# Performance work log

Measured on AMD Instinct MI355X. Metric: run time of the kernel, lower is better.

Reference implementation:

```python
import jax, jax.numpy as jnp
import numpy as np
from itertools import permutations as _permutations

N_ORB = 64
N_ALPHA = 5
N_BETA = 5
TEMP = 1.0
PERMS5 = jnp.asarray(np.array(list(_permutations(range(5))), dtype=np.int32))  # (120, 5)


def setup_inputs() -> dict:
    key = jax.random.key(0)
    ks = jax.random.split(key, 16)
    B = 8192
    s = 0.02
    inp = {
        "uniform_alpha": jax.random.uniform(ks[0], (B, N_ORB), dtype=jnp.float32),
        "uniform_beta": jax.random.uniform(ks[1], (B, N_ORB), dtype=jnp.float32),
        # learnable params
        "alpha_logits": jax.random.normal(ks[2], (N_ORB,), dtype=jnp.float32) * s,
        # alpha_to_beta: Linear(n_orb,128) -> SiLU -> Linear(128,64)
        "W1": jax.random.normal(ks[3], (N_ORB, 128), dtype=jnp.float32) * s,
        "b1": jnp.zeros((128,), jnp.float32),
        "W2": jax.random.normal(ks[4], (128, 64), dtype=jnp.float32) * s,
        "b2": jnp.zeros((64,), jnp.float32),
        # beta_conditioned_scorer: Linear(n_orb+64,256)->SiLU->Linear(256,256)->SiLU->Linear(256,n_orb)
        "V1": jax.random.normal(ks[5], (N_ORB + 64, 256), dtype=jnp.float32) * s,
        "c1": jnp.zeros((256,), jnp.float32),
        "V2": jax.random.normal(ks[6], (256, 256), dtype=jnp.float32) * s,
        "c2": jnp.zeros((256,), jnp.float32),
        "V3": jax.random.normal(ks[7], (256, N_ORB), dtype=jnp.float32) * s,
        "c3": jnp.zeros((N_ORB,), jnp.float32),
    }
    return inp


def _gumbel_topk(logits, uniform, k):
    """Straight-through Gumbel top-k mask. logits, uniform: (B, n)."""
    g = -jnp.log(-jnp.log(jnp.maximum(uniform, 1e-10)))
    perturbed = (logits + g) / TEMP
    _, top_idx = jax.lax.top_k(perturbed, k)                      # (B, k)
    B = logits.shape[0]
    one_hot = jnp.zeros_like(logits).at[jnp.arange(B)[:, None], top_idx].set(1.0)
    soft = jax.nn.softmax(perturbed, axis=-1)
    return one_hot - jax.lax.stop_gradient(soft) + soft


def _exact_pl_log_prob(logits, selection, k, perms):
    """log P(unordered top-k set) under Plackett-Luce, exact over k! orderings.

    logits: (B, n); selection: (B, n) soft/hard mask; perms: (P, k) static.
    """
    B, n = logits.shape
    P = perms.shape[0]
    _, sel_idx = jax.lax.top_k(selection, k)
    sel_idx = jnp.sort(sel_idx, axis=-1)                          # (B, k)
    perm_idx = sel_idx[:, perms]                                  # (B, P, k)
    lg = logits[:, None, :]                                       # (B, 1, n)
    remaining = jnp.ones((B, P, n), dtype=bool)
    lp = jnp.zeros((B, P), logits.dtype)
    bi = jnp.arange(B)[:, None]
    pi = jnp.arange(P)[None, :]
    for step in range(k):  # k is small and static (5)
        masked = jnp.where(remaining, lg, -jnp.inf)
        logp = jax.nn.log_softmax(masked, axis=-1)                # (B, P, n)
        idx = perm_idx[:, :, step]                                # (B, P)
        lp = lp + jnp.take_along_axis(logp, idx[..., None], axis=-1)[..., 0]
        remaining = remaining.at[bi, pi, idx].set(False)
    return jax.scipy.special.logsumexp(lp, axis=-1)              # (B,)


def reference(uniform_alpha, uniform_beta, alpha_logits, W1, b1, W2, b2,
              V1, c1, V2, c2, V3, c3):
    B = uniform_alpha.shape[0]
    a_logits = jnp.broadcast_to(alpha_logits[None, :], (B, N_ORB))
    alpha_config = _gumbel_topk(a_logits, uniform_alpha, N_ALPHA)

    # alpha_to_beta MLP
    h = jax.nn.silu(alpha_config @ W1 + b1)
    alpha_context = h @ W2 + b2                                   # (B, 64)

    beta_input = jnp.concatenate([jnp.zeros((B, N_ORB), a_logits.dtype), alpha_context], axis=-1)
    z = jax.nn.silu(beta_input @ V1 + c1)
    z = jax.nn.silu(z @ V2 + c2)
    beta_logits = z @ V3 + c3                                     # (B, n_orb)

    beta_config = _gumbel_topk(beta_logits, uniform_beta, N_BETA)
    configs = jnp.concatenate([alpha_config, beta_config], axis=-1)

    lp_a = _exact_pl_log_prob(a_logits, alpha_config, N_ALPHA, PERMS5)
    lp_b = _exact_pl_log_prob(beta_logits, beta_config, N_BETA, PERMS5)
    log_probs = lp_a + lp_b
    return configs, log_probs
```

## Files before the change

kernel.cpp:

```cpp
#include <hip/hip_runtime.h>
#include <math.h>

#define NTH 1024
#define KP 264
#define SPB 16
#define OFF_W2 0
#define OFF_V1 16384
#define OFF_V2 49152
#define OFF_V3 180224
#define WS_USHORTS 212992
#define MFMA16 __builtin_amdgcn_mfma_f32_16x16x32_bf16

typedef __attribute__((ext_vector_type(8))) short s16x8;
typedef __attribute__((ext_vector_type(8))) unsigned short u16x8;
typedef __attribute__((ext_vector_type(4))) float f32x4;

__device__ __forceinline__ float waveSum(float v) {
#pragma unroll
  for (int off = 32; off; off >>= 1) v += __shfl_xor(v, off, 64);
  return v;
}

__device__ __forceinline__ float siluf(float x) { return x / (1.0f + expf(-x)); }

__device__ __forceinline__ unsigned short bround(float x) {
  unsigned u = __float_as_uint(x);
  return (unsigned short)((u + 0x7FFFu + ((u >> 16) & 1u)) >> 16);
}

__device__ __forceinline__ void bsplit(float x, unsigned short& h, unsigned short& l) {
  unsigned u = __float_as_uint(x);
  unsigned hb = (u + 0x7FFFu + ((u >> 16) & 1u)) >> 16;
  float hf = __uint_as_float(hb << 16);
  float lf = x - hf;
  unsigned ul = __float_as_uint(lf);
  unsigned lb = (ul + 0x7FFFu + ((ul >> 16) & 1u)) >> 16;
  h = (unsigned short)hb; l = (unsigned short)lb;
}

__device__ __forceinline__ float permSum(const float se0, const float se1,
                                         const float se2, const float se3,
                                         const float se4, float Z, int lane) {
  float psum = 0.0f;
#pragma unroll
  for (int pp = 0; pp < 2; ++pp) {
    int p = lane + pp * 64;
    if (p < 120) {
      int rem = p;
      unsigned avail = 0x43210u;
      float c = 0.0f;
      float prod = Z;
#pragma unroll
      for (int j = 0; j < 4; ++j) {
        const int fct = (j == 0) ? 24 : (j == 1) ? 6 : (j == 2) ? 2 : 1;
        int q = rem / fct; rem -= q * fct;
        int sh = q * 4;
        int dg = (avail >> sh) & 0xF;
        avail = (avail & ((1u << sh) - 1u)) | ((avail >> (sh + 4)) << sh);
        float ev = (dg == 0) ? se0 : (dg == 1) ? se1 : (dg == 2) ? se2
                 : (dg == 3) ? se3 : se4;
        c += ev;
        prod *= (Z - c);
      }
      psum += 1.0f / prod;
    }
  }
  return psum;
}

__device__ __forceinline__ float selectAndPL(float lv, float ev, float Z,
                                             const float* __restrict__ u64,
                                             float* __restrict__ gout,
                                             int lane,
                                             float* __restrict__ sValsRow,
                                             float* __restrict__ sSelERow,
                                             int* __restrict__ selIdxRow) {
  float u = u64[lane];
  float g = -logf(-logf(fmaxf(u, 1e-10f)));
  float v = lv + g;
  sValsRow[lane] = v;
  int rank = 0;
#pragma unroll
  for (int j = 0; j < 16; ++j) {
    float4 w = *(const float4*)&sValsRow[j * 4];
    int base = j * 4;
    rank += (w.x > v || (w.x == v && base + 0 < lane)) ? 1 : 0;
    rank += (w.y > v || (w.y == v && base + 1 < lane)) ? 1 : 0;
    rank += (w.z > v || (w.z == v && base + 2 < lane)) ? 1 : 0;
    rank += (w.w > v || (w.w == v && base + 3 < lane)) ? 1 : 0;
  }
  bool sel = rank < 5;
  gout[lane] = sel ? 1.0f : 0.0f;
  if (sel) {
    sSelERow[rank] = ev;
    if (selIdxRow) selIdxRow[rank] = lane;
  }
  float sl = waveSum(sel ? lv : 0.0f);
  float se0 = sSelERow[0], se1 = sSelERow[1], se2 = sSelERow[2],
        se3 = sSelERow[3], se4 = sSelERow[4];
  float S = waveSum(permSum(se0, se1, se2, se3, se4, Z, lane));
  return sl + logf(S);
}

__global__ __launch_bounds__(256)
void pcf_prep(const float* __restrict__ W2, const float* __restrict__ V1,
              const float* __restrict__ V2, const float* __restrict__ V3,
              unsigned short* __restrict__ ws)
{
  int tid = blockIdx.x * 256 + threadIdx.x;
  const float* src; int N, Ks, dstoff, r;
  if (tid < 1024)       { src = W2;            N = 64;  Ks = 4; dstoff = OFF_W2; r = tid; }
  else if (tid < 3072)  { src = V1 + 64 * 256; N = 256; Ks = 2; dstoff = OFF_V1; r = tid - 1024; }
  else if (tid < 11264) { src = V2;            N = 256; Ks = 8; dstoff = OFF_V2; r = tid - 3072; }
  else                  { src = V3;            N = 64;  Ks = 8; dstoff = OFF_V3; r = tid - 11264; }
  int lane = r & 63, ts = r >> 6;
  int ks = ts % Ks, ct = ts / Ks;
  int n = ct * 16 + (lane & 15);
  int k0 = ks * 32 + (lane >> 4) * 8;
  u16x8 hv, lv;
#pragma unroll
  for (int j = 0; j < 8; ++j) {
    float x = src[(size_t)(k0 + j) * N + n];
    unsigned short h, l;
    bsplit(x, h, l);
    hv[j] = h; lv[j] = l;
  }
  unsigned short* dst = ws + dstoff + (size_t)ts * 1024 + lane * 8;
  *(u16x8*)dst = hv;
  *(u16x8*)(dst + 512) = lv;
}

__global__ __launch_bounds__(NTH, 8)
void pcf_mfma(const float* __restrict__ ua, const float* __restrict__ ub,
              const float* __restrict__ alog, const float* __restrict__ W1,
              const float* __restrict__ b1, const float* __restrict__ b2,
              const float* __restrict__ c1, const float* __restrict__ c2,
              const float* __restrict__ c3,
              const unsigned short* __restrict__ wt, float* __restrict__ out)
{
  __shared__ unsigned short sAhi[16 * KP];
  __shared__ unsigned short sBhi[16 * KP];
  __shared__ float sBL[SPB * 64];
  __shared__ float sVals[16 * 64];
  __shared__ float sSelE[16 * 8];
  __shared__ int   sSelA[SPB * 5];
  __shared__ float sLpA[SPB];

  const int t    = threadIdx.x;
  const int lane = t & 63;
  const int wv   = t >> 6;
  const int ln15 = lane & 15;
  const int quad = lane >> 4;
  const int bbase = blockIdx.x * SPB;

  float* sValsRow = &sVals[wv * 64];
  float* sSelERow = &sSelE[wv * 8];

  {
    float la = alog[lane];
    float ea = expf(la);
    float Za = waveSum(ea);
    int b = bbase + wv;
    float lp = selectAndPL(la, ea, Za, ua + (size_t)b * 64,
                           out + (size_t)b * 128, lane,
                           sValsRow, sSelERow, &sSelA[wv * 5]);
    if (lane == 0) sLpA[wv] = lp;
  }
  __syncthreads();

  {
    int s = wv;
    int j = lane * 2;
    const int rows[5] = { sSelA[s * 5 + 0], sSelA[s * 5 + 1], sSelA[s * 5 + 2],
                          sSelA[s * 5 + 3], sSelA[s * 5 + 4] };
    float2 a = *(const float2*)(b1 + j);
#pragma unroll
    for (int r = 0; r < 5; ++r) {
      float2 w = *(const float2*)(W1 + (size_t)rows[r] * 128 + j);
      a.x += w.x; a.y += w.y;
    }
    unsigned h0 = bround(siluf(a.x));
    unsigned h1 = bround(siluf(a.y));
    *(unsigned*)&sAhi[s * KP + j] = h0 | (h1 << 16);
  }
  __syncthreads();

  if (wv < 4) {
    f32x4 acc = {0.f, 0.f, 0.f, 0.f};
#pragma unroll
    for (int ks = 0; ks < 4; ++ks) {
      int ko = ks * 32 + quad * 8;
      s16x8 ah = *(const s16x8*)&sAhi[ln15 * KP + ko];
      const unsigned short* tsb = wt + OFF_W2 + (size_t)(wv * 4 + ks) * 1024;
      s16x8 bh = ((const s16x8*)tsb)[lane];
      s16x8 bl = ((const s16x8*)(tsb + 512))[lane];
      acc = MFMA16(ah, bh, acc, 0, 0, 0);
      acc = MFMA16(ah, bl, acc, 0, 0, 0);
    }
    int col = wv * 16 + ln15;
    float bias = b2[col];
#pragma unroll
    for (int r = 0; r < 4; ++r)
      sBhi[(quad * 4 + r) * KP + col] = bround(acc[r] + bias);
  }
  __syncthreads();

  {
    f32x4 acc = {0.f, 0.f, 0.f, 0.f};
#pragma unroll
    for (int ks = 0; ks < 2; ++ks) {
      int ko = ks * 32 + quad * 8;
      s16x8 ah = *(const s16x8*)&sBhi[ln15 * KP + ko];
      const unsigned short* tsb = wt + OFF_V1 + (size_t)(wv * 2 + ks) * 1024;
      s16x8 bh = ((const s16x8*)tsb)[lane];
      s16x8 bl = ((const s16x8*)(tsb + 512))[lane];
      acc = MFMA16(ah, bh, acc, 0, 0, 0);
      acc = MFMA16(ah, bl, acc, 0, 0, 0);
    }
    int col = wv * 16 + ln15;
    float bias = c1[col];
#pragma unroll
    for (int r = 0; r < 4; ++r)
      sAhi[(quad * 4 + r) * KP + col] = bround(siluf(acc[r] + bias));
  }
  __syncthreads();

  {
    f32x4 acc = {0.f, 0.f, 0.f, 0.f};
#pragma unroll 4
    for (int ks = 0; ks < 8; ++ks) {
      int ko = ks * 32 + quad * 8;
      s16x8 ah = *(const s16x8*)&sAhi[ln15 * KP + ko];
      const unsigned short* tsb = wt + OFF_V2 + (size_t)(wv * 8 + ks) * 1024;
      s16x8 bh = ((const s16x8*)tsb)[lane];
      s16x8 bl = ((const s16x8*)(tsb + 512))[lane];
      acc = MFMA16(ah, bh, acc, 0, 0, 0);
      acc = MFMA16(ah, bl, acc, 0, 0, 0);
    }
    int col = wv * 16 + ln15;
    float bias = c2[col];
#pragma unroll
    for (int r = 0; r < 4; ++r)
      sBhi[(quad * 4 + r) * KP + col] = bround(siluf(acc[r] + bias));
  }
  __syncthreads();

  if (wv < 4) {
    f32x4 acc = {0.f, 0.f, 0.f, 0.f};
#pragma unroll
    for (int ks = 0; ks < 8; ++ks) {
      int ko = ks * 32 + quad * 8;
      s16x8 ah = *(const s16x8*)&sBhi[ln15 * KP + ko];
      const unsigned short* tsb = wt + OFF_V3 + (size_t)(wv * 8 + ks) * 1024;
      s16x8 bh = ((const s16x8*)tsb)[lane];
      s16x8 bl = ((const s16x8*)(tsb + 512))[lane];
      acc = MFMA16(ah, bh, acc, 0, 0, 0);
      acc = MFMA16(ah, bl, acc, 0, 0, 0);
    }
    int col = wv * 16 + ln15;
    float bias = c3[col];
#pragma unroll
    for (int r = 0; r < 4; ++r)
      sBL[(quad * 4 + r) * 64 + col] = acc[r] + bias;
  }
  __syncthreads();

  {
    int b = bbase + wv;
    float blv = sBL[wv * 64 + lane];
    float eb = expf(blv);
    float Zb = waveSum(eb);
    float lp = selectAndPL(blv, eb, Zb, ub + (size_t)b * 64,
                           out + (size_t)b * 128 + 64, lane,
                           sValsRow, sSelERow, nullptr);
    if (lane == 0)
      out[(size_t)8192 * 128 + b] = sLpA[wv] + lp;
  }
}

#define SPB4 4
__global__ __launch_bounds__(256, 8)
void pcf_small(const float* __restrict__ ua, const float* __restrict__ ub,
               const float* __restrict__ alog, const float* __restrict__ W1,
               const float* __restrict__ b1, const float* __restrict__ W2,
               const float* __restrict__ b2, const float* __restrict__ V1,
               const float* __restrict__ c1, const float* __restrict__ V2,
               const float* __restrict__ c2, const float* __restrict__ V3,
               const float* __restrict__ c3, float* __restrict__ out)
{
  __shared__ float sA[SPB4 * 256];
  __shared__ float sB[SPB4 * 256];
  __shared__ float sP[4 * 256];
  __shared__ float sVals[4 * 64];
  __shared__ float sSelE[4 * 8];
  __shared__ int   sSelA[SPB4 * 5];
  __shared__ float sLpA[SPB4];

  const int t    = threadIdx.x;
  const int lane = t & 63;
  const int wv   = t >> 6;
  const int bbase = blockIdx.x * SPB4;

  float* sValsRow = &sVals[wv * 64];
  float* sSelERow = &sSelE[wv * 8];

  {
    float la = alog[lane];
    float ea = expf(la);
    float Za = waveSum(ea);
    int b = bbase + wv;
    float lp = selectAndPL(la, ea, Za, ua + (size_t)b * 64,
                           out + (size_t)b * 128, lane,
                           sValsRow, sSelERow, &sSelA[wv * 5]);
    if (lane == 0) sLpA[wv] = lp;
  }
  __syncthreads();
  {
    int s = wv;
    int i0 = sSelA[s * 5 + 0], i1 = sSelA[s * 5 + 1], i2 = sSelA[s * 5 + 2];
    int i3 = sSelA[s * 5 + 3], i4 = sSelA[s * 5 + 4];
#pragma unroll
    for (int jh = 0; jh < 2; ++jh) {
      int j = lane + jh * 64;
      float acc = b1[j] + W1[i0 * 128 + j] + W1[i1 * 128 + j]
                + W1[i2 * 128 + j] + W1[i3 * 128 + j] + W1[i4 * 128 + j];
      sA[s * 128 + j] = siluf(acc);
    }
  }
  __syncthreads();
  {
    float acc[SPB4] = {};
    const int kb = 32 * wv;
#pragma unroll 2
    for (int m = 0; m < 8; ++m) {
      int k0 = kb + 4 * m;
      float w0 = W2[(k0 + 0) * 64 + lane];
      float w1 = W2[(k0 + 1) * 64 + lane];
      float w2 = W2[(k0 + 2) * 64 + lane];
      float w3 = W2[(k0 + 3) * 64 + lane];
#pragma unroll
      for (int s = 0; s < SPB4; ++s) {
        float4 x = *(float4*)&sA[s * 128 + k0];
        acc[s] += x.x * w0 + x.y * w1 + x.z * w2 + x.w * w3;
      }
    }
#pragma unroll
    for (int s = 0; s < SPB4; ++s) sP[wv * 256 + s * 64 + lane] = acc[s];
  }
  __syncthreads();
  {
    int o = t;
    float v = b2[o & 63] + sP[o] + sP[256 + o] + sP[512 + o] + sP[768 + o];
    sB[o] = v;
  }
  __syncthreads();
  {
    const int c = 64 * wv + lane;
    float acc[SPB4];
    float cb = c1[c];
#pragma unroll
    for (int s = 0; s < SPB4; ++s) acc[s] = cb;
    const float* wp = V1 + (size_t)64 * 256 + c;
#pragma unroll 4
    for (int m = 0; m < 16; ++m) {
      int k0 = 4 * m;
      float w0 = wp[(k0 + 0) * 256];
      float w1 = wp[(k0 + 1) * 256];
      float w2 = wp[(k0 + 2) * 256];
      float w3 = wp[(k0 + 3) * 256];
#pragma unroll
      for (int s = 0; s < SPB4; ++s) {
        float4 x = *(float4*)&sB[s * 64 + k0];
        acc[s] += x.x * w0 + x.y * w1 + x.z * w2 + x.w * w3;
      }
    }
#pragma unroll
    for (int s = 0; s < SPB4; ++s) sA[s * 256 + c] = siluf(acc[s]);
  }
  __syncthreads();
  {
    const int c = 64 * wv + lane;
    float acc[SPB4];
    float cb = c2[c];
#pragma unroll
    for (int s = 0; s < SPB4; ++s) acc[s] = cb;
    const float* wp = V2 + c;
#pragma unroll 4
    for (int m = 0; m < 64; ++m) {
      int k0 = 4 * m;
      float w0 = wp[(size_t)(k0 + 0) * 256];
      float w1 = wp[(size_t)(k0 + 1) * 256];
      float w2 = wp[(size_t)(k0 + 2) * 256];
      float w3 = wp[(size_t)(k0 + 3) * 256];
#pragma unroll
      for (int s = 0; s < SPB4; ++s) {
        float4 x = *(float4*)&sA[s * 256 + k0];
        acc[s] += x.x * w0 + x.y * w1 + x.z * w2 + x.w * w3;
      }
    }
#pragma unroll
    for (int s = 0; s < SPB4; ++s) sB[s * 256 + c] = siluf(acc[s]);
  }
  __syncthreads();
  {
    float acc[SPB4] = {};
    const int kb = 64 * wv;
#pragma unroll 4
    for (int m = 0; m < 16; ++m) {
      int k0 = kb + 4 * m;
      float w0 = V3[(k0 + 0) * 64 + lane];
      float w1 = V3[(k0 + 1) * 64 + lane];
      float w2 = V3[(k0 + 2) * 64 + lane];
      float w3 = V3[(k0 + 3) * 64 + lane];
#pragma unroll
      for (int s = 0; s < SPB4; ++s) {
        float4 x = *(float4*)&sB[s * 256 + k0];
        acc[s] += x.x * w0 + x.y * w1 + x.z * w2 + x.w * w3;
      }
    }
#pragma unroll
    for (int s = 0; s < SPB4; ++s) sP[wv * 256 + s * 64 + lane] = acc[s];
  }
  __syncthreads();
  {
    int b = bbase + wv;
    float blv = c3[lane] + sP[wv * 64 + lane] + sP[256 + wv * 64 + lane]
              + sP[512 + wv * 64 + lane] + sP[768 + wv * 64 + lane];
    float eb = expf(blv);
    float Zb = waveSum(eb);
    float lp = selectAndPL(blv, eb, Zb, ub + (size_t)b * 64,
                           out + (size_t)b * 128 + 64, lane,
                           sValsRow, sSelERow, nullptr);
    if (lane == 0)
      out[(size_t)8192 * 128 + b] = sLpA[wv] + lp;
  }
}

extern "C" void kernel_launch(void* const* d_in, const int* in_sizes, int n_in,
                              void* d_out, int out_size, void* d_ws, size_t ws_size,
                              hipStream_t stream) {
  const float* ua   = (const float*)d_in[0];
  const float* ub   = (const float*)d_in[1];
  const float* alog = (const float*)d_in[2];
  const float* W1   = (const float*)d_in[3];
  const float* b1   = (const float*)d_in[4];
  const float* W2   = (const float*)d_in[5];
  const float* b2   = (const float*)d_in[6];
  const float* V1   = (const float*)d_in[7];
  const float* c1   = (const float*)d_in[8];
  const float* V2   = (const float*)d_in[9];
  const float* c2   = (const float*)d_in[10];
  const float* V3   = (const float*)d_in[11];
  const float* c3   = (const float*)d_in[12];
  float* out = (float*)d_out;

  if (ws_size >= (size_t)WS_USHORTS * 2) {
    unsigned short* wt = (unsigned short*)d_ws;
    pcf_prep<<<dim3(52), dim3(256), 0, stream>>>(W2, V1, V2, V3, wt);
    pcf_mfma<<<dim3(8192 / SPB), dim3(NTH), 0, stream>>>(
        ua, ub, alog, W1, b1, b2, c1, c2, c3, wt, out);
  } else {
    pcf_small<<<dim3(8192 / SPB4), dim3(256), 0, stream>>>(
        ua, ub, alog, W1, b1, W2, b2, V1, c1, V2, c2, V3, c3, out);
  }
}
```

Baseline: 108.3 us.

## Halve block to 512 threads, two samples per wave, prefetch beta uniforms

The MFMA kernel's block drops from 16 to 8 waves. Each wave now handles two samples in the selection stages and two 16-column tiles in the V1 and V2 GEMM stages. The beta uniforms are loaded and their Gumbel noise computed at kernel start, so that global load latency overlaps the MLP work. This cuts per-block barrier cost and lets more blocks share a CU, but each wave carries more serial work and more registers. The W2 and V3 stages still use wv<4, which now means half of the 8 waves.

```diff
diff --git a/kernel.cpp b/kernel.cpp
--- a/kernel.cpp
+++ b/kernel.cpp
@@ -1,7 +1,7 @@
 #include <hip/hip_runtime.h>
 #include <math.h>
 
-#define NTH 1024
+#define NTH 512
 #define KP 264
 #define SPB 16
 #define OFF_W2 0
@@ -69,14 +69,12 @@
 }
 
 __device__ __forceinline__ float selectAndPL(float lv, float ev, float Z,
-                                             const float* __restrict__ u64,
+                                             float g,
                                              float* __restrict__ gout,
                                              int lane,
                                              float* __restrict__ sValsRow,
                                              float* __restrict__ sSelERow,
                                              int* __restrict__ selIdxRow) {
-  float u = u64[lane];
-  float g = -logf(-logf(fmaxf(u, 1e-10f)));
   float v = lv + g;
   sValsRow[lane] = v;
   int rank = 0;
@@ -141,8 +139,8 @@
   __shared__ unsigned short sAhi[16 * KP];
   __shared__ unsigned short sBhi[16 * KP];
   __shared__ float sBL[SPB * 64];
-  __shared__ float sVals[16 * 64];
-  __shared__ float sSelE[16 * 8];
+  __shared__ float sVals[SPB * 64];
+  __shared__ float sSelE[SPB * 8];
   __shared__ int   sSelA[SPB * 5];
   __shared__ float sLpA[SPB];
 
@@ -153,35 +151,49 @@
   const int quad = lane >> 4;
   const int bbase = blockIdx.x * SPB;
 
-  float* sValsRow = &sVals[wv * 64];
-  float* sSelERow = &sSelE[wv * 8];
+  float gb[2];
+#pragma unroll
+  for (int si = 0; si < 2; ++si) {
+    int b = bbase + wv * 2 + si;
+    float u = ub[(size_t)b * 64 + lane];
+    gb[si] = -logf(-logf(fmaxf(u, 1e-10f)));
+  }
 
   {
     float la = alog[lane];
     float ea = expf(la);
     float Za = waveSum(ea);
-    int b = bbase + wv;
-    float lp = selectAndPL(la, ea, Za, ua + (size_t)b * 64,
-                           out + (size_t)b * 128, lane,
-                           sValsRow, sSelERow, &sSelA[wv * 5]);
-    if (lane == 0) sLpA[wv] = lp;
-  }
-  __syncthreads();
-
-  {
-    int s = wv;
+#pragma unroll
+    for (int si = 0; si < 2; ++si) {
+      int s = wv * 2 + si;
+      int b = bbase + s;
+      float u = ua[(size_t)b * 64 + lane];
+      float ga = -logf(-logf(fmaxf(u, 1e-10f)));
+      float lp = selectAndPL(la, ea, Za, ga, out + (size_t)b * 128, lane,
+                             &sVals[s * 64], &sSelE[s * 8], &sSelA[s * 5]);
+      if (lane == 0) sLpA[s] = lp;
+    }
+  }
+  __syncthreads();
+
+  {
     int j = lane * 2;
-    const int rows[5] = { sSelA[s * 5 + 0], sSelA[s * 5 + 1], sSelA[s * 5 + 2],
-                          sSelA[s * 5 + 3], sSelA[s * 5 + 4] };
-    float2 a = *(const float2*)(b1 + j);
-#pragma unroll
-    for (int r = 0; r < 5; ++r) {
-      float2 w = *(const float2*)(W1 + (size_t)rows[r] * 128 + j);
-      a.x += w.x; a.y += w.y;
-    }
-    unsigned h0 = bround(siluf(a.x));
-    unsigned h1 = bround(siluf(a.y));
-    *(unsigned*)&sAhi[s * KP + j] = h0 | (h1 << 16);
+    float2 bv = *(const float2*)(b1 + j);
+#pragma unroll
+    for (int si = 0; si < 2; ++si) {
+      int s = wv * 2 + si;
+      const int rows[5] = { sSelA[s * 5 + 0], sSelA[s * 5 + 1], sSelA[s * 5 + 2],
+                            sSelA[s * 5 + 3], sSelA[s * 5 + 4] };
+      float2 a = bv;
+#pragma unroll
+      for (int r = 0; r < 5; ++r) {
+        float2 w = *(const float2*)(W1 + (size_t)rows[r] * 128 + j);
+        a.x += w.x; a.y += w.y;
+      }
+      unsigned h0 = bround(siluf(a.x));
+      unsigned h1 = bround(siluf(a.y));
+      *(unsigned*)&sAhi[s * KP + j] = h0 | (h1 << 16);
+    }
   }
   __syncthreads();
 
@@ -206,42 +218,58 @@
   __syncthreads();
 
   {
-    f32x4 acc = {0.f, 0.f, 0.f, 0.f};
+    f32x4 acc[2];
+#pragma unroll
+    for (int i = 0; i < 2; ++i) acc[i] = (f32x4){0.f, 0.f, 0.f, 0.f};
 #pragma unroll
     for (int ks = 0; ks < 2; ++ks) {
       int ko = ks * 32 + quad * 8;
       s16x8 ah = *(const s16x8*)&sBhi[ln15 * KP + ko];
-      const unsigned short* tsb = wt + OFF_V1 + (size_t)(wv * 2 + ks) * 1024;
-      s16x8 bh = ((const s16x8*)tsb)[lane];
-      s16x8 bl = ((const s16x8*)(tsb + 512))[lane];
-      acc = MFMA16(ah, bh, acc, 0, 0, 0);
-      acc = MFMA16(ah, bl, acc, 0, 0, 0);
-    }
-    int col = wv * 16 + ln15;
-    float bias = c1[col];
-#pragma unroll
-    for (int r = 0; r < 4; ++r)
-      sAhi[(quad * 4 + r) * KP + col] = bround(siluf(acc[r] + bias));
-  }
-  __syncthreads();
-
-  {
-    f32x4 acc = {0.f, 0.f, 0.f, 0.f};
+#pragma unroll
+      for (int i = 0; i < 2; ++i) {
+        const unsigned short* tsb = wt + OFF_V1 + (size_t)((wv * 2 + i) * 2 + ks) * 1024;
+        s16x8 bh = ((const s16x8*)tsb)[lane];
+        s16x8 bl = ((const s16x8*)(tsb + 512))[lane];
+        acc[i] = MFMA16(ah, bh, acc[i], 0, 0, 0);
+        acc[i] = MFMA16(ah, bl, acc[i], 0, 0, 0);
+      }
+    }
+#pragma unroll
+    for (int i = 0; i < 2; ++i) {
+      int col = (wv * 2 + i) * 16 + ln15;
+      float bias = c1[col];
+#pragma unroll
+      for (int r = 0; r < 4; ++r)
+        sAhi[(quad * 4 + r) * KP + col] = bround(siluf(acc[i][r] + bias));
+    }
+  }
+  __syncthreads();
+
+  {
+    f32x4 acc[2];
+#pragma unroll
+    for (int i = 0; i < 2; ++i) acc[i] = (f32x4){0.f, 0.f, 0.f, 0.f};
 #pragma unroll 4
     for (int ks = 0; ks < 8; ++ks) {
       int ko = ks * 32 + quad * 8;
       s16x8 ah = *(const s16x8*)&sAhi[ln15 * KP + ko];
-      const unsigned short* tsb = wt + OFF_V2 + (size_t)(wv * 8 + ks) * 1024;
-      s16x8 bh = ((const s16x8*)tsb)[lane];
-      s16x8 bl = ((const s16x8*)(tsb + 512))[lane];
-      acc = MFMA16(ah, bh, acc, 0, 0, 0);
-      acc = MFMA16(ah, bl, acc, 0, 0, 0);
-    }
-    int col = wv * 16 + ln15;
-    float bias = c2[col];
-#pragma unroll
-    for (int r = 0; r < 4; ++r)
-      sBhi[(quad * 4 + r) * KP + col] = bround(siluf(acc[r] + bias));
+#pragma unroll
+      for (int i = 0; i < 2; ++i) {
+        const unsigned short* tsb = wt + OFF_V2 + (size_t)((wv * 2 + i) * 8 + ks) * 1024;
+        s16x8 bh = ((const s16x8*)tsb)[lane];
+        s16x8 bl = ((const s16x8*)(tsb + 512))[lane];
+        acc[i] = MFMA16(ah, bh, acc[i], 0, 0, 0);
+        acc[i] = MFMA16(ah, bl, acc[i], 0, 0, 0);
+      }
+    }
+#pragma unroll
+    for (int i = 0; i < 2; ++i) {
+      int col = (wv * 2 + i) * 16 + ln15;
+      float bias = c2[col];
+#pragma unroll
+      for (int r = 0; r < 4; ++r)
+        sBhi[(quad * 4 + r) * KP + col] = bround(siluf(acc[i][r] + bias));
+    }
   }
   __syncthreads();
 
@@ -266,15 +294,19 @@
   __syncthreads();
 
   {
-    int b = bbase + wv;
-    float blv = sBL[wv * 64 + lane];
-    float eb = expf(blv);
-    float Zb = waveSum(eb);
-    float lp = selectAndPL(blv, eb, Zb, ub + (size_t)b * 64,
-                           out + (size_t)b * 128 + 64, lane,
-                           sValsRow, sSelERow, nullptr);
-    if (lane == 0)
-      out[(size_t)8192 * 128 + b] = sLpA[wv] + lp;
+#pragma unroll
+    for (int si = 0; si < 2; ++si) {
+      int s = wv * 2 + si;
+      int b = bbase + s;
+      float blv = sBL[s * 64 + lane];
+      float eb = expf(blv);
+      float Zb = waveSum(eb);
+      float lp = selectAndPL(blv, eb, Zb, gb[si],
+                             out + (size_t)b * 128 + 64, lane,
+                             &sVals[s * 64], &sSelE[s * 8], nullptr);
+      if (lane == 0)
+        out[(size_t)8192 * 128 + b] = sLpA[s] + lp;
+    }
   }
 }
 
@@ -309,8 +341,9 @@
     float ea = expf(la);
     float Za = waveSum(ea);
     int b = bbase + wv;
-    float lp = selectAndPL(la, ea, Za, ua + (size_t)b * 64,
-                           out + (size_t)b * 128, lane,
+    float u = ua[(size_t)b * 64 + lane];
+    float g = -logf(-logf(fmaxf(u, 1e-10f)));
+    float lp = selectAndPL(la, ea, Za, g, out + (size_t)b * 128, lane,
                            sValsRow, sSelERow, &sSelA[wv * 5]);
     if (lane == 0) sLpA[wv] = lp;
   }
@@ -428,8 +461,9 @@
               + sP[512 + wv * 64 + lane] + sP[768 + wv * 64 + lane];
     float eb = expf(blv);
     float Zb = waveSum(eb);
-    float lp = selectAndPL(blv, eb, Zb, ub + (size_t)b * 64,
-                           out + (size_t)b * 128 + 64, lane,
+    float u = ub[(size_t)b * 64 + lane];
+    float g = -logf(-logf(fmaxf(u, 1e-10f)));
+    float lp = selectAndPL(blv, eb, Zb, g, out + (size_t)b * 128 + 64, lane,
                            sValsRow, sSelERow, nullptr);
     if (lane == 0)
       out[(size_t)8192 * 128 + b] = sLpA[wv] + lp;
```

New measurement: 118.3 us. +9.3%, slower.
